# Kernel optimization log

Hardware: AMD Instinct MI355X
Metric: run time of the kernel (lower is better)

Reference implementation:

```python
import jax, jax.numpy as jnp
import numpy as np

N_NODES = 2_000_000
D_FEAT = 64
NUM_SEGMENTS = 8192


def setup_inputs() -> dict:
    key = jax.random.key(0)
    k_feat, k_batch = jax.random.split(key)
    # Values near 1.0 so long products neither underflow nor overflow.
    feats = 0.99 + 0.02 * jax.random.uniform(k_feat, (N_NODES, D_FEAT), dtype=jnp.float32)
    batch = jnp.sort(jax.random.randint(k_batch, (N_NODES,), 0, NUM_SEGMENTS, dtype=jnp.int64))
    return {"feats": feats, "batch": batch}


def reference(feats, batch):
    # scatter_mul(feats, batch, dim=0): per-segment elementwise product.
    # Empty segments default to 1 (multiplicative identity), matching torch_scatter.
    return jax.ops.segment_prod(feats, batch, num_segments=NUM_SEGMENTS)
```

## Files before the change

kernel.cpp:

```cpp
#include <hip/hip_runtime.h>
#include <hip/hip_bf16.h>


__global__ __launch_bounds__(256) void bounds_kernel(
    const int* __restrict__ batch,
    int*       __restrict__ seg_start,
    int n_nodes, int num_segments)
{
    const int s = blockIdx.x * blockDim.x + threadIdx.x;
    if (s > num_segments) return;
    if (s == num_segments) { seg_start[s] = n_nodes; return; }
    if (s == 0)            { seg_start[0] = 0;       return; }

    int lo = 0, hi = n_nodes;
    while (lo < hi) {
        int mid = (lo + hi) >> 1;
        if (batch[mid] < s) lo = mid + 1; else hi = mid;
    }
    seg_start[s] = lo;
}

__global__ __launch_bounds__(256) void prod_kernel(
    const float4* __restrict__ feats,
    const int*    __restrict__ seg_start,
    float4*       __restrict__ out)
{
    const int s     = blockIdx.x;
    const int start = seg_start[s];
    const int end   = seg_start[s + 1];

    const int tid  = threadIdx.x;
    const int quad = tid & 15;
    const int rofs = tid >> 4;

    float4 acc = make_float4(1.0f, 1.0f, 1.0f, 1.0f);
    for (int r = start + rofs; r < end; r += 16) {
        float4 v = feats[(size_t)r * 16 + quad];
        acc.x *= v.x; acc.y *= v.y; acc.z *= v.z; acc.w *= v.w;
    }

    __shared__ float4 lds[256];
    lds[tid] = acc;
    __syncthreads();

    #pragma unroll
    for (int step = 128; step >= 16; step >>= 1) {
        if (tid < step) {
            float4 o = lds[tid + step];
            float4 m = lds[tid];
            m.x *= o.x; m.y *= o.y; m.z *= o.z; m.w *= o.w;
            lds[tid] = m;
        }
        __syncthreads();
    }

    if (tid < 16) {
        out[(size_t)s * 16 + tid] = lds[tid];
    }
}

extern "C" void kernel_launch(void* const* d_in, const int* in_sizes, int n_in,
                              void* d_out, int out_size, void* d_ws, size_t ws_size,
                              hipStream_t stream) {
    const float4* feats = (const float4*)d_in[0];
    const int*    batch = (const int*)d_in[1];
    float4*       out   = (float4*)d_out;
    int*          seg_start = (int*)d_ws;

    const int n_nodes      = in_sizes[0] / 64;
    const int num_segments = out_size   / 64;

    const int nb = (num_segments + 1 + 255) / 256;
    bounds_kernel<<<nb, 256, 0, stream>>>(batch, seg_start, n_nodes, num_segments);
    prod_kernel<<<num_segments, 256, 0, stream>>>(feats, seg_start, out);
}
```

Baseline: 103.6 us.

## Use one wavefront per segment with shuffle reduction and boundary-scan bounds

Replaces the per-segment binary search with a linear scan over the sorted batch array, where each node writes the segment starts at its boundaries. The product kernel now gives each segment one 64-lane wavefront instead of a 256-thread block. It uses two independent accumulators, nontemporal vector loads and xor-shuffle reduction in place of LDS and __syncthreads. Each segment holds about 244 rows of 64 floats, so the intent is to cut block-level sync overhead and raise memory-level parallelism per wave. The scan reads all 2M batch entries instead of doing about 8K log-depth searches, and nb_prod assumes num_segments*64 divides by 256.

```diff
diff --git a/kernel.cpp b/kernel.cpp
--- a/kernel.cpp
+++ b/kernel.cpp
@@ -2,75 +2,79 @@
 #include <hip/hip_bf16.h>
 
 
-__global__ __launch_bounds__(256) void bounds_kernel(
+typedef float f32x4 __attribute__((ext_vector_type(4)));
+
+__global__ __launch_bounds__(256) void bounds_scan_kernel(
     const int* __restrict__ batch,
     int*       __restrict__ seg_start,
     int n_nodes, int num_segments)
 {
-    const int s = blockIdx.x * blockDim.x + threadIdx.x;
-    if (s > num_segments) return;
-    if (s == num_segments) { seg_start[s] = n_nodes; return; }
-    if (s == 0)            { seg_start[0] = 0;       return; }
-
-    int lo = 0, hi = n_nodes;
-    while (lo < hi) {
-        int mid = (lo + hi) >> 1;
-        if (batch[mid] < s) lo = mid + 1; else hi = mid;
+    const int i = blockIdx.x * blockDim.x + threadIdx.x;
+    if (i >= n_nodes) return;
+    const int b0 = batch[i];
+    const int b1 = (i + 1 < n_nodes) ? batch[i + 1] : num_segments;
+    if (i == 0) {
+        for (int s = 0; s <= b0; ++s) seg_start[s] = 0;
     }
-    seg_start[s] = lo;
+    for (int s = b0 + 1; s <= b1; ++s) seg_start[s] = i + 1;
 }
 
 __global__ __launch_bounds__(256) void prod_kernel(
-    const float4* __restrict__ feats,
-    const int*    __restrict__ seg_start,
-    float4*       __restrict__ out)
+    const f32x4* __restrict__ feats,
+    const int*   __restrict__ seg_start,
+    f32x4*       __restrict__ out)
 {
-    const int s     = blockIdx.x;
+    const int gtid = blockIdx.x * 256 + threadIdx.x;
+    const int s    = gtid >> 6;
+    const int lane = gtid & 63;
+    const int quad = lane & 15;
+    const int rofs = lane >> 4;
+
     const int start = seg_start[s];
     const int end   = seg_start[s + 1];
 
-    const int tid  = threadIdx.x;
-    const int quad = tid & 15;
-    const int rofs = tid >> 4;
+    f32x4 a0 = {1.f, 1.f, 1.f, 1.f};
+    f32x4 a1 = {1.f, 1.f, 1.f, 1.f};
 
-    float4 acc = make_float4(1.0f, 1.0f, 1.0f, 1.0f);
-    for (int r = start + rofs; r < end; r += 16) {
-        float4 v = feats[(size_t)r * 16 + quad];
-        acc.x *= v.x; acc.y *= v.y; acc.z *= v.z; acc.w *= v.w;
+    int r = start + rofs;
+    for (; r + 4 < end; r += 8) {
+        f32x4 v0 = __builtin_nontemporal_load(&feats[(size_t)r       * 16 + quad]);
+        f32x4 v1 = __builtin_nontemporal_load(&feats[(size_t)(r + 4) * 16 + quad]);
+        a0 *= v0;
+        a1 *= v1;
     }
+    if (r < end) {
+        a0 *= __builtin_nontemporal_load(&feats[(size_t)r * 16 + quad]);
+    }
+    a0 *= a1;
 
-    __shared__ float4 lds[256];
-    lds[tid] = acc;
-    __syncthreads();
+    f32x4 t;
+    t.x = __shfl_xor(a0.x, 16); t.y = __shfl_xor(a0.y, 16);
+    t.z = __shfl_xor(a0.z, 16); t.w = __shfl_xor(a0.w, 16);
+    a0 *= t;
+    t.x = __shfl_xor(a0.x, 32); t.y = __shfl_xor(a0.y, 32);
+    t.z = __shfl_xor(a0.z, 32); t.w = __shfl_xor(a0.w, 32);
+    a0 *= t;
 
-    #pragma unroll
-    for (int step = 128; step >= 16; step >>= 1) {
-        if (tid < step) {
-            float4 o = lds[tid + step];
-            float4 m = lds[tid];
-            m.x *= o.x; m.y *= o.y; m.z *= o.z; m.w *= o.w;
-            lds[tid] = m;
-        }
-        __syncthreads();
-    }
-
-    if (tid < 16) {
-        out[(size_t)s * 16 + tid] = lds[tid];
+    if (lane < 16) {
+        out[(size_t)s * 16 + quad] = a0;
     }
 }
 
 extern "C" void kernel_launch(void* const* d_in, const int* in_sizes, int n_in,
                               void* d_out, int out_size, void* d_ws, size_t ws_size,
                               hipStream_t stream) {
-    const float4* feats = (const float4*)d_in[0];
-    const int*    batch = (const int*)d_in[1];
-    float4*       out   = (float4*)d_out;
-    int*          seg_start = (int*)d_ws;
+    const f32x4* feats = (const f32x4*)d_in[0];
+    const int*   batch = (const int*)d_in[1];
+    f32x4*       out   = (f32x4*)d_out;
+    int*         seg_start = (int*)d_ws;
 
     const int n_nodes      = in_sizes[0] / 64;
     const int num_segments = out_size   / 64;
 
-    const int nb = (num_segments + 1 + 255) / 256;
-    bounds_kernel<<<nb, 256, 0, stream>>>(batch, seg_start, n_nodes, num_segments);
-    prod_kernel<<<num_segments, 256, 0, stream>>>(feats, seg_start, out);
+    const int nb_scan = (n_nodes + 255) / 256;
+    bounds_scan_kernel<<<nb_scan, 256, 0, stream>>>(batch, seg_start, n_nodes, num_segments);
+
+    const int nb_prod = (num_segments * 64) / 256;
+    prod_kernel<<<nb_prod, 256, 0, stream>>>(feats, seg_start, out);
 }
```

Result: faster. 94.26 us (-9.0%).
